# Kernel optimization log

Hardware: AMD Instinct MI355X
Metric: run time of the kernel (lower is better)

## Reference

```python
import jax, jax.numpy as jnp
import numpy as np

BIN_SIZE = 256
TOP_K = 16


def setup_inputs() -> dict:
    key = jax.random.key(0)
    kx, kc = jax.random.split(key)
    x = jax.random.normal(kx, (2, 4096, 512), dtype=jnp.float32)
    codebook = jax.random.normal(kc, (512, 16), dtype=jnp.float32)  # (feature_dim, max_num_bins//2)
    return {"x": x, "codebook": codebook}


def reference(x, codebook):
    B, N, F = x.shape
    n_bins = N // BIN_SIZE  # 16
    # LSH bucket assignment: project onto random hyperplanes, pick argmax of [p, -p]
    mul = x @ codebook[:, : n_bins // 2]                      # (B, N, n_bins//2)
    cmul = jnp.concatenate([mul, -mul], axis=-1)              # (B, N, n_bins)
    bin_idx = jnp.argmax(cmul, axis=-1)                       # (B, N)
    # argsort-based binning: equal-size bins of points sorted by bucket id
    bins_split = jnp.argsort(bin_idx, axis=-1).reshape(B, n_bins, BIN_SIZE)
    # gather points into bins: (B, n_bins, bin_size, F)
    points_binned = jnp.take_along_axis(x[:, None, :, :], bins_split[..., None], axis=2)
    # intra-bin dense similarity + sigmoid
    dm = jax.nn.sigmoid(jnp.einsum('bnif,bnjf->bnij', points_binned, points_binned))
    vals, idx = jax.lax.top_k(dm, TOP_K)                      # (B, n_bins, bin_size, k)
    # map local bin indices back to global point indices
    dst = jnp.take_along_axis(bins_split[:, :, None, :], idx, axis=-1)  # (B, nb, bs, k)
    src = jnp.broadcast_to(bins_split[..., None], dst.shape)
    b = jnp.broadcast_to(jnp.arange(B)[:, None, None, None], dst.shape)
    # dense equivalent of the coalesced batched sparse_coo_tensor of size (N, N)
    out = jnp.zeros((B, N, N), dtype=x.dtype).at[b, src, dst].add(vals)
    return out
```

## Files before the change

kernel.cpp:

```cpp
#include <hip/hip_runtime.h>
#include <stdint.h>
#include <math.h>

#define NPTS 4096
#define NF 512
#define NBINS 16
#define BSZ 256
#define TOPK 16
#define NBATCH 2
#define SPART (NBATCH * NBINS * BSZ * BSZ)

typedef float vf4 __attribute__((ext_vector_type(4)));

__global__ __launch_bounds__(256) void k_assign(const float* __restrict__ x,
                                                const float* __restrict__ cb,
                                                int* __restrict__ bin_idx) {
    int gw   = (blockIdx.x * 256 + threadIdx.x) >> 6;
    int lane = threadIdx.x & 63;
    const float* row = x + (size_t)gw * NF;
    float acc[8];
#pragma unroll
    for (int j = 0; j < 8; j++) acc[j] = 0.f;
    for (int f = lane; f < NF; f += 64) {
        float xv = row[f];
        const float4* c = (const float4*)(cb + f * 16);
        float4 c0 = c[0], c1 = c[1];
        acc[0] += xv * c0.x; acc[1] += xv * c0.y; acc[2] += xv * c0.z; acc[3] += xv * c0.w;
        acc[4] += xv * c1.x; acc[5] += xv * c1.y; acc[6] += xv * c1.z; acc[7] += xv * c1.w;
    }
#pragma unroll
    for (int off = 32; off > 0; off >>= 1) {
#pragma unroll
        for (int j = 0; j < 8; j++) acc[j] += __shfl_xor(acc[j], off, 64);
    }
    if (lane == 0) {
        float best = acc[0]; int bi = 0;
#pragma unroll
        for (int j = 1; j < 8; j++) { if (acc[j] > best) { best = acc[j]; bi = j; } }
#pragma unroll
        for (int j = 0; j < 8; j++) { float v = -acc[j]; if (v > best) { best = v; bi = 8 + j; } }
        bin_idx[gw] = bi;
    }
}

__global__ __launch_bounds__(256) void k_sort(const int* __restrict__ bin_idx,
                                              int* __restrict__ order) {
    __shared__ int hist[NBINS][256];
    __shared__ int segsum[NBINS][16];
    __shared__ int segoff[NBINS][16];
    __shared__ int totals[NBINS];
    __shared__ int keybase[NBINS];
    int b = blockIdx.x, t = threadIdx.x;
    const int* bi = bin_idx + b * NPTS;
#pragma unroll
    for (int j = 0; j < NBINS; j++) hist[j][t] = 0;
    int base = t * 16;
    for (int i = 0; i < 16; i++) { int k = bi[base + i]; hist[k][t]++; }
    __syncthreads();
    {
        int j = t >> 4, sg = t & 15, s = 0;
#pragma unroll
        for (int u = 0; u < 16; u++) s += hist[j][sg * 16 + u];
        segsum[j][sg] = s;
    }
    __syncthreads();
    if (t < NBINS) {
        int run = 0;
#pragma unroll
        for (int sg = 0; sg < 16; sg++) { int c = segsum[t][sg]; segoff[t][sg] = run; run += c; }
        totals[t] = run;
    }
    __syncthreads();
    if (t == 0) {
        int run = 0;
#pragma unroll
        for (int j = 0; j < NBINS; j++) { keybase[j] = run; run += totals[j]; }
    }
    __syncthreads();
    {
        int j = t >> 4, sg = t & 15;
        int run = segoff[j][sg];
#pragma unroll
        for (int u = 0; u < 16; u++) { int c = hist[j][sg * 16 + u]; hist[j][sg * 16 + u] = run; run += c; }
    }
    __syncthreads();
    int* ob = order + b * NPTS;
    for (int i = 0; i < 16; i++) {
        int k = bi[base + i];
        int o = hist[k][t];
        hist[k][t] = o + 1;
        ob[keybase[k] + o] = base + i;
    }
}

__global__ __launch_bounds__(256, 2) void k_gemm(const float* __restrict__ x,
                                                 const int* __restrict__ order,
                                                 float* __restrict__ S) {
    int blk = blockIdx.x;
    int kh  = blk & 3;
    int tn  = (blk >> 2) & 1;
    int tm  = (blk >> 3) & 1;
    int bin = (blk >> 4) & 15;
    int b   = blk >> 8;
    int t  = threadIdx.x;
    int tx = t & 15, ty = t >> 4;
    __shared__ int   idxA[128];
    __shared__ int   idxB[128];
    __shared__ float Asl[32][132];
    __shared__ float Bsl[32][132];
    int ob = b * NPTS + bin * BSZ;
    if (t < 128) idxA[t] = order[ob + tm * 128 + t];
    else         idxB[t - 128] = order[ob + tn * 128 + (t - 128)];
    __syncthreads();
    const float* xb = x + (size_t)b * (NPTS * NF);
    int rowi = t & 127;
    int qb   = t >> 7;
    const float* rowA = xb + (size_t)idxA[rowi] * NF + kh * 128;
    const float* rowB = xb + (size_t)idxB[rowi] * NF + kh * 128;
    float acc[8][8];
#pragma unroll
    for (int i = 0; i < 8; i++)
#pragma unroll
        for (int j = 0; j < 8; j++) acc[i][j] = 0.f;
    float4 pa[4], pb[4];
#pragma unroll
    for (int l = 0; l < 4; l++) {
        pa[l] = *(const float4*)(rowA + (qb + 2 * l) * 4);
        pb[l] = *(const float4*)(rowB + (qb + 2 * l) * 4);
    }
    for (int it = 0; it < 4; it++) {
        __syncthreads();
#pragma unroll
        for (int l = 0; l < 4; l++) {
            int kq = (qb + 2 * l) * 4;
            Asl[kq + 0][rowi] = pa[l].x; Asl[kq + 1][rowi] = pa[l].y;
            Asl[kq + 2][rowi] = pa[l].z; Asl[kq + 3][rowi] = pa[l].w;
            Bsl[kq + 0][rowi] = pb[l].x; Bsl[kq + 1][rowi] = pb[l].y;
            Bsl[kq + 2][rowi] = pb[l].z; Bsl[kq + 3][rowi] = pb[l].w;
        }
        __syncthreads();
        if (it < 3) {
            const float* a2 = rowA + (it + 1) * 32;
            const float* b2 = rowB + (it + 1) * 32;
#pragma unroll
            for (int l = 0; l < 4; l++) {
                pa[l] = *(const float4*)(a2 + (qb + 2 * l) * 4);
                pb[l] = *(const float4*)(b2 + (qb + 2 * l) * 4);
            }
        }
#pragma unroll
        for (int kk = 0; kk < 32; kk++) {
            float4 a0 = *(const float4*)&Asl[kk][ty * 8];
            float4 a1 = *(const float4*)&Asl[kk][ty * 8 + 4];
            float4 b0 = *(const float4*)&Bsl[kk][tx * 8];
            float4 b1 = *(const float4*)&Bsl[kk][tx * 8 + 4];
            float av[8] = {a0.x, a0.y, a0.z, a0.w, a1.x, a1.y, a1.z, a1.w};
            float bv[8] = {b0.x, b0.y, b0.z, b0.w, b1.x, b1.y, b1.z, b1.w};
#pragma unroll
            for (int i = 0; i < 8; i++)
#pragma unroll
                for (int j = 0; j < 8; j++) acc[i][j] += av[i] * bv[j];
        }
    }
    float* Sp = S + (size_t)kh * SPART;
    size_t rowbase = (size_t)(b * NBINS + bin) * BSZ;
#pragma unroll
    for (int i = 0; i < 8; i++) {
        int r = tm * 128 + ty * 8 + i;
        float* orow = Sp + (rowbase + r) * BSZ + tn * 128 + tx * 8;
        *(float4*)(orow)     = make_float4(acc[i][0], acc[i][1], acc[i][2], acc[i][3]);
        *(float4*)(orow + 4) = make_float4(acc[i][4], acc[i][5], acc[i][6], acc[i][7]);
    }
}

__global__ __launch_bounds__(64) void k_topkw(const float* __restrict__ S,
                                              const int* __restrict__ order,
                                              float* __restrict__ out) {
    __shared__ float buf[NPTS];
    int row  = blockIdx.x;
    int lane = threadIdx.x;
    const float* s0 = S + (size_t)row * BSZ;
    unsigned long long key[4];
#pragma unroll
    for (int q = 0; q < 4; q++) {
        int j = lane + 64 * q;
        float d = s0[j] + s0[j + SPART] + s0[j + 2 * SPART] + s0[j + 3 * SPART];
        float v = 1.0f / (1.0f + expf(-d));
        key[q] = ((unsigned long long)__float_as_uint(v) << 32) | (unsigned)(255 - j);
    }
    int   wj[TOPK];
    float wv[TOPK];
#pragma unroll
    for (int it = 0; it < TOPK; it++) {
        unsigned long long k = key[0];
        if (key[1] > k) k = key[1];
        if (key[2] > k) k = key[2];
        if (key[3] > k) k = key[3];
#pragma unroll
        for (int off = 32; off > 0; off >>= 1) {
            unsigned long long o = __shfl_xor(k, off, 64);
            if (o > k) k = o;
        }
        int jw = 255 - (int)(k & 0xFFull);
        wj[it] = jw;
        wv[it] = __uint_as_float((unsigned)(k >> 32));
        if ((jw & 63) == lane) {
            int q = jw >> 6;
            if      (q == 0) key[0] = 0ull;
            else if (q == 1) key[1] = 0ull;
            else if (q == 2) key[2] = 0ull;
            else             key[3] = 0ull;
        }
    }
    vf4 z = {0.f, 0.f, 0.f, 0.f};
#pragma unroll
    for (int u = 0; u < 16; u++) ((vf4*)buf)[u * 64 + lane] = z;
    int b   = row >> 12;
    int bin = (row >> 8) & 15;
    int i   = row & 255;
    const int* obp = order + b * NPTS + bin * BSZ;
    int srcg = obp[i];
    __syncthreads();
#pragma unroll
    for (int it = 0; it < TOPK; it++) {
        if (lane == it) buf[obp[wj[it]]] = wv[it];
    }
    __syncthreads();
    vf4* orow = (vf4*)(out + ((size_t)b * NPTS + srcg) * NPTS);
#pragma unroll
    for (int u = 0; u < 16; u++) {
        __builtin_nontemporal_store(((const vf4*)buf)[u * 64 + lane], &orow[u * 64 + lane]);
    }
}

extern "C" void kernel_launch(void* const* d_in, const int* in_sizes, int n_in,
                              void* d_out, int out_size, void* d_ws, size_t ws_size,
                              hipStream_t stream) {
    const float* x  = (const float*)d_in[0];
    const float* cb = (const float*)d_in[1];
    float* out = (float*)d_out;
    int*   bin_idx = (int*)d_ws;
    int*   order   = bin_idx + NBATCH * NPTS;
    float* S       = (float*)d_ws + 4 * NBATCH * NPTS;

    k_assign<<<2048, 256, 0, stream>>>(x, cb, bin_idx);
    k_sort  <<<NBATCH, 256, 0, stream>>>(bin_idx, order);
    k_gemm  <<<512, 256, 0, stream>>>(x, order, S);
    k_topkw <<<NBATCH * NPTS * NBINS / 16, 64, 0, stream>>>(S, order, out);
}
```

Measured before the change: 208.9 us.

## Parallelize sort per key, swizzle GEMM LDS layout, vectorize top-k loads

Result: slower. 230.9 us (+10.6%).

```diff
diff --git a/kernel.cpp b/kernel.cpp
--- a/kernel.cpp
+++ b/kernel.cpp
@@ -9,8 +9,11 @@
 #define TOPK 16
 #define NBATCH 2
 #define SPART (NBATCH * NBINS * BSZ * BSZ)
+#define SA 164
 
 typedef float vf4 __attribute__((ext_vector_type(4)));
+
+__device__ __forceinline__ int sw(int c) { return c + ((c >> 4) << 2); }
 
 __global__ __launch_bounds__(256) void k_assign(const float* __restrict__ x,
                                                 const float* __restrict__ cb,
@@ -45,51 +48,34 @@
 
 __global__ __launch_bounds__(256) void k_sort(const int* __restrict__ bin_idx,
                                               int* __restrict__ order) {
-    __shared__ int hist[NBINS][256];
-    __shared__ int segsum[NBINS][16];
-    __shared__ int segoff[NBINS][16];
-    __shared__ int totals[NBINS];
-    __shared__ int keybase[NBINS];
-    int b = blockIdx.x, t = threadIdx.x;
+    __shared__ int s_eq[256];
+    __shared__ int s_lt[256];
+    int b   = blockIdx.x >> 4;
+    int key = blockIdx.x & 15;
+    int t   = threadIdx.x;
     const int* bi = bin_idx + b * NPTS;
-#pragma unroll
-    for (int j = 0; j < NBINS; j++) hist[j][t] = 0;
     int base = t * 16;
-    for (int i = 0; i < 16; i++) { int k = bi[base + i]; hist[k][t]++; }
-    __syncthreads();
-    {
-        int j = t >> 4, sg = t & 15, s = 0;
-#pragma unroll
-        for (int u = 0; u < 16; u++) s += hist[j][sg * 16 + u];
-        segsum[j][sg] = s;
-    }
-    __syncthreads();
-    if (t < NBINS) {
-        int run = 0;
-#pragma unroll
-        for (int sg = 0; sg < 16; sg++) { int c = segsum[t][sg]; segoff[t][sg] = run; run += c; }
-        totals[t] = run;
-    }
-    __syncthreads();
-    if (t == 0) {
-        int run = 0;
-#pragma unroll
-        for (int j = 0; j < NBINS; j++) { keybase[j] = run; run += totals[j]; }
-    }
-    __syncthreads();
-    {
-        int j = t >> 4, sg = t & 15;
-        int run = segoff[j][sg];
-#pragma unroll
-        for (int u = 0; u < 16; u++) { int c = hist[j][sg * 16 + u]; hist[j][sg * 16 + u] = run; run += c; }
-    }
-    __syncthreads();
-    int* ob = order + b * NPTS;
+    int e[16];
+    { const int4* p = (const int4*)(bi + base);
+      int4 a0 = p[0], a1 = p[1], a2 = p[2], a3 = p[3];
+      e[0]=a0.x; e[1]=a0.y; e[2]=a0.z; e[3]=a0.w;
+      e[4]=a1.x; e[5]=a1.y; e[6]=a1.z; e[7]=a1.w;
+      e[8]=a2.x; e[9]=a2.y; e[10]=a2.z; e[11]=a2.w;
+      e[12]=a3.x; e[13]=a3.y; e[14]=a3.z; e[15]=a3.w; }
+    int ceq = 0, clt = 0;
+#pragma unroll
+    for (int i = 0; i < 16; i++) { ceq += (e[i] == key); clt += (e[i] < key); }
+    s_eq[t] = ceq; s_lt[t] = clt;
+    __syncthreads();
+    int keybase = 0, myoff = 0;
+    for (int u = 0; u < 256; u++) {
+        keybase += s_lt[u];
+        if (u < t) myoff += s_eq[u];
+    }
+    int* ob = order + b * NPTS + keybase;
+#pragma unroll
     for (int i = 0; i < 16; i++) {
-        int k = bi[base + i];
-        int o = hist[k][t];
-        hist[k][t] = o + 1;
-        ob[keybase[k] + o] = base + i;
+        if (e[i] == key) ob[myoff++] = base + i;
     }
 }
 
@@ -106,8 +92,8 @@
     int tx = t & 15, ty = t >> 4;
     __shared__ int   idxA[128];
     __shared__ int   idxB[128];
-    __shared__ float Asl[32][132];
-    __shared__ float Bsl[32][132];
+    __shared__ float Asl[32 * SA];
+    __shared__ float Bsl[32 * SA];
     int ob = b * NPTS + bin * BSZ;
     if (t < 128) idxA[t] = order[ob + tm * 128 + t];
     else         idxB[t - 128] = order[ob + tn * 128 + (t - 128)];
@@ -115,6 +101,9 @@
     const float* xb = x + (size_t)b * (NPTS * NF);
     int rowi = t & 127;
     int qb   = t >> 7;
+    int swr  = sw(rowi);
+    int swA  = sw(ty * 8);
+    int swB  = sw(tx * 8);
     const float* rowA = xb + (size_t)idxA[rowi] * NF + kh * 128;
     const float* rowB = xb + (size_t)idxB[rowi] * NF + kh * 128;
     float acc[8][8];
@@ -133,10 +122,10 @@
 #pragma unroll
         for (int l = 0; l < 4; l++) {
             int kq = (qb + 2 * l) * 4;
-            Asl[kq + 0][rowi] = pa[l].x; Asl[kq + 1][rowi] = pa[l].y;
-            Asl[kq + 2][rowi] = pa[l].z; Asl[kq + 3][rowi] = pa[l].w;
-            Bsl[kq + 0][rowi] = pb[l].x; Bsl[kq + 1][rowi] = pb[l].y;
-            Bsl[kq + 2][rowi] = pb[l].z; Bsl[kq + 3][rowi] = pb[l].w;
+            Asl[(kq + 0) * SA + swr] = pa[l].x; Asl[(kq + 1) * SA + swr] = pa[l].y;
+            Asl[(kq + 2) * SA + swr] = pa[l].z; Asl[(kq + 3) * SA + swr] = pa[l].w;
+            Bsl[(kq + 0) * SA + swr] = pb[l].x; Bsl[(kq + 1) * SA + swr] = pb[l].y;
+            Bsl[(kq + 2) * SA + swr] = pb[l].z; Bsl[(kq + 3) * SA + swr] = pb[l].w;
         }
         __syncthreads();
         if (it < 3) {
@@ -150,10 +139,10 @@
         }
 #pragma unroll
         for (int kk = 0; kk < 32; kk++) {
-            float4 a0 = *(const float4*)&Asl[kk][ty * 8];
-            float4 a1 = *(const float4*)&Asl[kk][ty * 8 + 4];
-            float4 b0 = *(const float4*)&Bsl[kk][tx * 8];
-            float4 b1 = *(const float4*)&Bsl[kk][tx * 8 + 4];
+            float4 a0 = *(const float4*)&Asl[kk * SA + swA];
+            float4 a1 = *(const float4*)&Asl[kk * SA + swA + 4];
+            float4 b0 = *(const float4*)&Bsl[kk * SA + swB];
+            float4 b1 = *(const float4*)&Bsl[kk * SA + swB + 4];
             float av[8] = {a0.x, a0.y, a0.z, a0.w, a1.x, a1.y, a1.z, a1.w};
             float bv[8] = {b0.x, b0.y, b0.z, b0.w, b1.x, b1.y, b1.z, b1.w};
 #pragma unroll
@@ -180,13 +169,17 @@
     int row  = blockIdx.x;
     int lane = threadIdx.x;
     const float* s0 = S + (size_t)row * BSZ;
+    vf4 v0 = *(const vf4*)&s0[4 * lane];
+    vf4 v1 = *(const vf4*)&s0[4 * lane + SPART];
+    vf4 v2 = *(const vf4*)&s0[4 * lane + 2 * SPART];
+    vf4 v3 = *(const vf4*)&s0[4 * lane + 3 * SPART];
     unsigned long long key[4];
 #pragma unroll
-    for (int q = 0; q < 4; q++) {
-        int j = lane + 64 * q;
-        float d = s0[j] + s0[j + SPART] + s0[j + 2 * SPART] + s0[j + 3 * SPART];
+    for (int c = 0; c < 4; c++) {
+        int j = 4 * lane + c;
+        float d = v0[c] + v1[c] + v2[c] + v3[c];
         float v = 1.0f / (1.0f + expf(-d));
-        key[q] = ((unsigned long long)__float_as_uint(v) << 32) | (unsigned)(255 - j);
+        key[c] = ((unsigned long long)__float_as_uint(v) << 32) | (unsigned)(255 - j);
     }
     int   wj[TOPK];
     float wv[TOPK];
@@ -204,11 +197,11 @@
         int jw = 255 - (int)(k & 0xFFull);
         wj[it] = jw;
         wv[it] = __uint_as_float((unsigned)(k >> 32));
-        if ((jw & 63) == lane) {
-            int q = jw >> 6;
-            if      (q == 0) key[0] = 0ull;
-            else if (q == 1) key[1] = 0ull;
-            else if (q == 2) key[2] = 0ull;
+        if ((jw >> 2) == lane) {
+            int c = jw & 3;
+            if      (c == 0) key[0] = 0ull;
+            else if (c == 1) key[1] = 0ull;
+            else if (c == 2) key[2] = 0ull;
             else             key[3] = 0ull;
         }
     }
@@ -244,7 +237,7 @@
     float* S       = (float*)d_ws + 4 * NBATCH * NPTS;
 
     k_assign<<<2048, 256, 0, stream>>>(x, cb, bin_idx);
-    k_sort  <<<NBATCH, 256, 0, stream>>>(bin_idx, order);
+    k_sort  <<<NBATCH * NBINS, 256, 0, stream>>>(bin_idx, order);
     k_gemm  <<<512, 256, 0, stream>>>(x, order, S);
     k_topkw <<<NBATCH * NPTS * NBINS / 16, 64, 0, stream>>>(S, order, out);
 }
```

## Zero output in GEMM launch and scatter only top-k values afterwards

Applied to the files above, without the earlier changes.

After: 226.4 us. 8.4% more time.

```diff
diff --git a/kernel.cpp b/kernel.cpp
--- a/kernel.cpp
+++ b/kernel.cpp
@@ -9,6 +9,7 @@
 #define TOPK 16
 #define NBATCH 2
 #define SPART (NBATCH * NBINS * BSZ * BSZ)
+#define NZERO 2048
 
 typedef float vf4 __attribute__((ext_vector_type(4)));
 
@@ -93,21 +94,31 @@
     }
 }
 
-__global__ __launch_bounds__(256, 2) void k_gemm(const float* __restrict__ x,
-                                                 const int* __restrict__ order,
-                                                 float* __restrict__ S) {
-    int blk = blockIdx.x;
+__global__ __launch_bounds__(256, 2) void k_gemmzero(const float* __restrict__ x,
+                                                     const int* __restrict__ order,
+                                                     float* __restrict__ S,
+                                                     float* __restrict__ out) {
+    __shared__ int   idxA[128];
+    __shared__ int   idxB[128];
+    __shared__ float Asl[32][132];
+    __shared__ float Bsl[32][132];
+    int t = threadIdx.x;
+    if (blockIdx.x < NZERO) {
+        vf4 z = {0.f, 0.f, 0.f, 0.f};
+        vf4* p = (vf4*)out + (size_t)blockIdx.x * 4096;
+#pragma unroll
+        for (int u = 0; u < 16; u++) {
+            __builtin_nontemporal_store(z, &p[u * 256 + t]);
+        }
+        return;
+    }
+    int blk = blockIdx.x - NZERO;
     int kh  = blk & 3;
     int tn  = (blk >> 2) & 1;
     int tm  = (blk >> 3) & 1;
     int bin = (blk >> 4) & 15;
     int b   = blk >> 8;
-    int t  = threadIdx.x;
     int tx = t & 15, ty = t >> 4;
-    __shared__ int   idxA[128];
-    __shared__ int   idxB[128];
-    __shared__ float Asl[32][132];
-    __shared__ float Bsl[32][132];
     int ob = b * NPTS + bin * BSZ;
     if (t < 128) idxA[t] = order[ob + tm * 128 + t];
     else         idxB[t - 128] = order[ob + tn * 128 + (t - 128)];
@@ -173,10 +184,9 @@
     }
 }
 
-__global__ __launch_bounds__(64) void k_topkw(const float* __restrict__ S,
+__global__ __launch_bounds__(64) void k_patch(const float* __restrict__ S,
                                               const int* __restrict__ order,
                                               float* __restrict__ out) {
-    __shared__ float buf[NPTS];
     int row  = blockIdx.x;
     int lane = threadIdx.x;
     const float* s0 = S + (size_t)row * BSZ;
@@ -188,8 +198,7 @@
         float v = 1.0f / (1.0f + expf(-d));
         key[q] = ((unsigned long long)__float_as_uint(v) << 32) | (unsigned)(255 - j);
     }
-    int   wj[TOPK];
-    float wv[TOPK];
+    int myj = 0; float myv = 0.f;
 #pragma unroll
     for (int it = 0; it < TOPK; it++) {
         unsigned long long k = key[0];
@@ -202,8 +211,7 @@
             if (o > k) k = o;
         }
         int jw = 255 - (int)(k & 0xFFull);
-        wj[it] = jw;
-        wv[it] = __uint_as_float((unsigned)(k >> 32));
+        if (lane == it) { myj = jw; myv = __uint_as_float((unsigned)(k >> 32)); }
         if ((jw & 63) == lane) {
             int q = jw >> 6;
             if      (q == 0) key[0] = 0ull;
@@ -212,24 +220,14 @@
             else             key[3] = 0ull;
         }
     }
-    vf4 z = {0.f, 0.f, 0.f, 0.f};
-#pragma unroll
-    for (int u = 0; u < 16; u++) ((vf4*)buf)[u * 64 + lane] = z;
     int b   = row >> 12;
     int bin = (row >> 8) & 15;
     int i   = row & 255;
     const int* obp = order + b * NPTS + bin * BSZ;
     int srcg = obp[i];
-    __syncthreads();
-#pragma unroll
-    for (int it = 0; it < TOPK; it++) {
-        if (lane == it) buf[obp[wj[it]]] = wv[it];
-    }
-    __syncthreads();
-    vf4* orow = (vf4*)(out + ((size_t)b * NPTS + srcg) * NPTS);
-#pragma unroll
-    for (int u = 0; u < 16; u++) {
-        __builtin_nontemporal_store(((const vf4*)buf)[u * 64 + lane], &orow[u * 64 + lane]);
+    if (lane < TOPK) {
+        int dstg = obp[myj];
+        out[((size_t)b * NPTS + srcg) * NPTS + dstg] = myv;
     }
 }
 
@@ -243,8 +241,8 @@
     int*   order   = bin_idx + NBATCH * NPTS;
     float* S       = (float*)d_ws + 4 * NBATCH * NPTS;
 
-    k_assign<<<2048, 256, 0, stream>>>(x, cb, bin_idx);
-    k_sort  <<<NBATCH, 256, 0, stream>>>(bin_idx, order);
-    k_gemm  <<<512, 256, 0, stream>>>(x, order, S);
-    k_topkw <<<NBATCH * NPTS * NBINS / 16, 64, 0, stream>>>(S, order, out);
-}
+    k_assign  <<<2048, 256, 0, stream>>>(x, cb, bin_idx);
+    k_sort    <<<NBATCH, 256, 0, stream>>>(bin_idx, order);
+    k_gemmzero<<<NZERO + 512, 256, 0, stream>>>(x, order, S, out);
+    k_patch   <<<NBATCH * NPTS * NBINS / 16, 64, 0, stream>>>(S, order, out);
+}
```
